# Performance work log

Measured on AMD Instinct MI355X. Metric: run time of the kernel, lower is better.

## Reference

```python
import jax, jax.numpy as jnp
import numpy as np

EMBED_DIM = 1024
NUM_HEADS = 16
HEAD_DIM = EMBED_DIM // NUM_HEADS
B, T = 4, 2048


def setup_inputs() -> dict:
    key = jax.random.key(0)
    ks = jax.random.split(key, 11)
    s = 1.0 / np.sqrt(EMBED_DIM)
    return {
        "query": jax.random.normal(ks[0], (B, T, EMBED_DIM), jnp.float32),
        "key_in": jax.random.normal(ks[1], (B, T, EMBED_DIM), jnp.float32),
        "value": jax.random.normal(ks[2], (B, T, EMBED_DIM), jnp.float32),
        "Wq": jax.random.normal(ks[3], (EMBED_DIM, EMBED_DIM), jnp.float32) * s,
        "bq": jnp.zeros((EMBED_DIM,), jnp.float32),
        "Wk": jax.random.normal(ks[4], (EMBED_DIM, EMBED_DIM), jnp.float32) * s,
        "bk": jnp.zeros((EMBED_DIM,), jnp.float32),
        "Wv": jax.random.normal(ks[5], (EMBED_DIM, EMBED_DIM), jnp.float32) * s,
        "bv": jnp.zeros((EMBED_DIM,), jnp.float32),
        "Wo": jax.random.normal(ks[6], (EMBED_DIM, EMBED_DIM), jnp.float32) * s,
        "bo": jnp.zeros((EMBED_DIM,), jnp.float32),
    }


def reference(query, key_in, value, Wq, bq, Wk, bk, Wv, bv, Wo, bo):
    # nn.Linear: x @ W.T + b
    def split_heads(x):  # [B,T,D] -> [B,H,T,hd]
        return x.reshape(B, T, NUM_HEADS, HEAD_DIM).transpose(0, 2, 1, 3)

    q = split_heads(query @ Wq.T + bq)
    k = split_heads(key_in @ Wk.T + bk)
    v = split_heads(value @ Wv.T + bv)
    scores = jnp.einsum("bhqd,bhkd->bhqk", q, k) / jnp.sqrt(jnp.float32(HEAD_DIM))
    attn = jax.nn.softmax(scores, axis=-1)
    out = jnp.einsum("bhqk,bhkd->bhqd", attn, v)
    out = out.transpose(0, 2, 1, 3).reshape(B, T, EMBED_DIM)
    return out @ Wo.T + bo
```

## Files before the change

kernel.cpp:

```cpp
#include <hip/hip_runtime.h>
#include <hip/hip_bf16.h>
#include <stdint.h>

typedef __bf16 bf16;
typedef __bf16 bf16x8 __attribute__((ext_vector_type(8)));
typedef float f32x4 __attribute__((ext_vector_type(4)));
typedef float f32x16 __attribute__((ext_vector_type(16)));

#define BATCH 4
#define SEQ   2048
#define DIM   1024
#define NH    16
#define HD    64

#define QSCALE 0.18033688011112042f

#define MFMA(a, b, c)   __builtin_amdgcn_mfma_f32_16x16x32_bf16((a), (b), (c), 0, 0, 0)
#define MFMA32(a, b, c) __builtin_amdgcn_mfma_f32_32x32x16_bf16((a), (b), (c), 0, 0, 0)

#define GLOAD16(gsrc, ldst)                                                        \
  __builtin_amdgcn_global_load_lds(                                                \
      (__attribute__((address_space(1))) unsigned int*)(void*)(gsrc),              \
      (__attribute__((address_space(3))) unsigned int*)(ldst), 16, 0, 0)

static __device__ __forceinline__ float fast_exp2(float x) {
#if __has_builtin(__builtin_amdgcn_exp2f)
  return __builtin_amdgcn_exp2f(x);
#else
  return exp2f(x);
#endif
}

__global__ __launch_bounds__(256) void cvt_w_kernel(
    const float* __restrict__ w0, const float* __restrict__ w1,
    const float* __restrict__ w2, const float* __restrict__ w3,
    bf16* __restrict__ o0, bf16* __restrict__ o1,
    bf16* __restrict__ o2, bf16* __restrict__ o3) {
  const float* s;
  bf16* d;
  switch (blockIdx.y) {
    case 0: s = w0; d = o0; break;
    case 1: s = w1; d = o1; break;
    case 2: s = w2; d = o2; break;
    default: s = w3; d = o3; break;
  }
  const int i = (blockIdx.x * 256 + threadIdx.x) * 4;
  const float4 v = *(const float4*)(s + i);
  ushort4 o;
  o.x = __builtin_bit_cast(unsigned short, (bf16)v.x);
  o.y = __builtin_bit_cast(unsigned short, (bf16)v.y);
  o.z = __builtin_bit_cast(unsigned short, (bf16)v.z);
  o.w = __builtin_bit_cast(unsigned short, (bf16)v.w);
  *(ushort4*)((unsigned short*)d + i) = o;
}

__global__ __launch_bounds__(256) void cvt_x_kernel(
    const float* __restrict__ in, bf16* __restrict__ out) {
  const int i = (blockIdx.x * 256 + threadIdx.x) * 8;
  const float4 v0 = *(const float4*)(in + i);
  const float4 v1 = *(const float4*)(in + i + 4);
  bf16x8 p;
  p[0] = (bf16)v0.x; p[1] = (bf16)v0.y; p[2] = (bf16)v0.z; p[3] = (bf16)v0.w;
  p[4] = (bf16)v1.x; p[5] = (bf16)v1.y; p[6] = (bf16)v1.z; p[7] = (bf16)v1.w;
  *(bf16x8*)(out + i) = p;
}

__global__ __launch_bounds__(256, 2) void proj_gemm(
    const bf16* __restrict__ A, const bf16* __restrict__ W,
    const float* __restrict__ bias, bf16* __restrict__ out, int z) {
  __shared__ bf16 Ab[2][128 * 64];
  __shared__ bf16 Bb[2][128 * 64];

  const int tid  = threadIdx.x;
  const int wave = tid >> 6, lane = tid & 63;
  const int r = lane & 15, g = lane >> 4;

  const int wg = blockIdx.x;
  const int sw = ((wg & 7) << 6) | (wg >> 3);
  const int m0 = (sw >> 3) * 128, n0 = (sw & 7) * 128;
  const int wm = (wave >> 1) * 64, wn = (wave & 1) * 64;

  f32x4 acc[4][4] = {};

  const int srr = lane >> 3;
  const int scb = (lane & 7) * 16;
  const int swz = srr << 4;

#define STAGEP(buf, k0)                                                             \
  do {                                                                              \
    _Pragma("unroll") for (int i_ = 0; i_ < 4; ++i_) {                              \
      const int row_ = wave * 32 + i_ * 8 + srr;                                    \
      const char* as_ =                                                             \
          (const char*)(A + (size_t)(m0 + row_) * DIM + (k0)) + (scb ^ swz);        \
      GLOAD16(as_, (char*)&Ab[buf][0] + (wave * 32 + i_ * 8) * 128);                \
      const char* bs_ =                                                             \
          (const char*)(W + (size_t)(n0 + row_) * DIM + (k0)) + (scb ^ swz);        \
      GLOAD16(bs_, (char*)&Bb[buf][0] + (wave * 32 + i_ * 8) * 128);                \
    }                                                                               \
  } while (0)

  STAGEP(0, 0);
  __syncthreads();

  const int NK = DIM / 64;
  for (int it = 0; it < NK; ++it) {
    const int cur = it & 1;
    if (it + 1 < NK) STAGEP(cur ^ 1, (it + 1) * 64);

#pragma unroll
    for (int ks = 0; ks < 2; ++ks) {
      bf16x8 af[4], bfr[4];
#pragma unroll
      for (int mt = 0; mt < 4; ++mt) {
        const int mr = wm + mt * 16 + r;
        af[mt] = *(bf16x8*)((char*)&Ab[cur][0] + mr * 128 +
                            ((ks * 64 + g * 16) ^ ((mr & 7) << 4)));
      }
#pragma unroll
      for (int nt = 0; nt < 4; ++nt) {
        const int nr = wn + nt * 16 + r;
        bfr[nt] = *(bf16x8*)((char*)&Bb[cur][0] + nr * 128 +
                             ((ks * 64 + g * 16) ^ ((nr & 7) << 4)));
      }
#pragma unroll
      for (int mt = 0; mt < 4; ++mt)
#pragma unroll
        for (int nt = 0; nt < 4; ++nt)
          acc[mt][nt] = MFMA(af[mt], bfr[nt], acc[mt][nt]);
    }

    __syncthreads();
  }
#undef STAGEP

  if (z == 2) {
#pragma unroll
    for (int nt = 0; nt < 4; ++nt) {
      const int n = n0 + wn + nt * 16 + r;
      const float bn = bias[n];
#pragma unroll
      for (int mt = 0; mt < 4; ++mt) {
        const int m = m0 + wm + mt * 16 + g * 4;
        const int b = m >> 11, t = m & 2047;
        ushort4 pk;
        pk.x = __builtin_bit_cast(unsigned short, (bf16)(acc[mt][nt][0] + bn));
        pk.y = __builtin_bit_cast(unsigned short, (bf16)(acc[mt][nt][1] + bn));
        pk.z = __builtin_bit_cast(unsigned short, (bf16)(acc[mt][nt][2] + bn));
        pk.w = __builtin_bit_cast(unsigned short, (bf16)(acc[mt][nt][3] + bn));
        *(ushort4*)((unsigned short*)out + (((size_t)(b * DIM + n)) << 11) + t) = pk;
      }
    }
  } else {
    const float scale = (z == 0) ? QSCALE : 1.0f;
#pragma unroll
    for (int mt = 0; mt < 4; ++mt)
#pragma unroll
      for (int nt = 0; nt < 4; ++nt) {
        const int n = n0 + wn + nt * 16 + r;
        const float bn = bias[n];
#pragma unroll
        for (int i = 0; i < 4; ++i) {
          const int m = m0 + wm + mt * 16 + g * 4 + i;
          out[(size_t)m * DIM + n] = (bf16)((acc[mt][nt][i] + bn) * scale);
        }
      }
  }
}

__global__ __launch_bounds__(256, 4) void attn_kernel(
    const bf16* __restrict__ Q, const bf16* __restrict__ K,
    const bf16* __restrict__ Vt, bf16* __restrict__ ctx) {
  __shared__ bf16 Kb[2][64 * 64];
  __shared__ bf16 Vb[2][64 * 64];

  const int tid  = threadIdx.x;
  const int wave = tid >> 6, lane = tid & 63;
  const int l31 = lane & 31, hi = lane >> 5;

  const int wg  = blockIdx.x;
  const int swb = (wg & 7) * 128 + (wg >> 3);
  const int qblk = swb & 15, bh = swb >> 4;
  const int b = bh >> 4, h = bh & 15;
  const int q0 = qblk * 128 + wave * 32;

  bf16x8 qf[4];
  {
    const bf16* qp = Q + ((size_t)(b * SEQ + q0 + l31) * DIM + h * HD);
#pragma unroll
    for (int st = 0; st < 4; ++st)
      qf[st] = *(const bf16x8*)(qp + st * 16 + hi * 8);
  }

  f32x16 accO[2] = {};
  float m_i = -3e38f, l_i = 0.0f;

  const bf16* Kbase = K + (size_t)(b * SEQ) * DIM + h * HD;
  const bf16* Vbase = Vt + (size_t)(b * DIM + h * HD) * SEQ;

  const int srr = lane >> 3;
  const int scb = (lane & 7) * 16;
  const int swz = srr << 4;

  int koff[2], voff[2], kdst[2], vdst[2];
#pragma unroll
  for (int i = 0; i < 2; ++i) {
    const int rl = wave * 16 + i * 8 + srr;
    const int r32 = rl & 31;
    const int t = (r32 >> 2) & 3;
    const int rsrc = (rl & 32) + ((t == 1 || t == 2) ? (r32 ^ 12) : r32);
    koff[i] = rsrc * (DIM * 2) + (scb ^ swz);
    voff[i] = rl * (SEQ * 2) + (scb ^ swz);
    kdst[i] = (wave * 16 + i * 8) * 128;
    vdst[i] = (wave * 16 + i * 8) * 128;
  }

#define STAGE(buf, kv0)                                                             \
  do {                                                                              \
    _Pragma("unroll") for (int i_ = 0; i_ < 2; ++i_) {                              \
      GLOAD16((const char*)Kbase + (size_t)(kv0) * (DIM * 2) + koff[i_],            \
              (char*)&Kb[buf][0] + kdst[i_]);                                       \
      GLOAD16((const char*)Vbase + (size_t)(kv0) * 2 + voff[i_],                    \
              (char*)&Vb[buf][0] + vdst[i_]);                                       \
    }                                                                               \
  } while (0)

  STAGE(0, 0);
  __syncthreads();

  const int NIT = SEQ / 64;
  for (int it = 0; it < NIT; ++it) {
    const int cur = it & 1;
    if (it + 1 < NIT) STAGE(cur ^ 1, (it + 1) * 64);

    f32x16 s[2] = {};
    __builtin_amdgcn_s_setprio(1);
#pragma unroll
    for (int kvt = 0; kvt < 2; ++kvt) {
      const int row = kvt * 32 + l31;
      const char* kb = (const char*)&Kb[cur][0] + row * 128;
      const int rsw = (row & 7) << 4;
#pragma unroll
      for (int st = 0; st < 4; ++st) {
        const bf16x8 kf = *(const bf16x8*)(kb + ((st * 32 + hi * 16) ^ rsw));
        s[kvt] = MFMA32(kf, qf[st], s[kvt]);
      }
    }
    __builtin_amdgcn_s_setprio(0);

    float pm = s[0][0];
#pragma unroll
    for (int kvt = 0; kvt < 2; ++kvt)
#pragma unroll
      for (int e = 0; e < 16; ++e)
        if (kvt || e) pm = fmaxf(pm, s[kvt][e]);
    pm = fmaxf(pm, __shfl_xor(pm, 32));

    if (__any(pm > m_i + 8.0f)) {
      const float mn = fmaxf(m_i, pm);
      const float alpha = fast_exp2(m_i - mn);
      m_i = mn;
      l_i *= alpha;
#pragma unroll
      for (int dt = 0; dt < 2; ++dt)
#pragma unroll
        for (int e = 0; e < 16; ++e) accO[dt][e] *= alpha;
    }

    float rs = 0.0f;
#pragma unroll
    for (int kvt = 0; kvt < 2; ++kvt)
#pragma unroll
      for (int e = 0; e < 16; ++e) {
        s[kvt][e] = fast_exp2(s[kvt][e] - m_i);
        rs += s[kvt][e];
      }
    l_i += rs + __shfl_xor(rs, 32);

    bf16x8 pa[2][2];
#pragma unroll
    for (int kvt = 0; kvt < 2; ++kvt)
#pragma unroll
      for (int kb = 0; kb < 2; ++kb)
#pragma unroll
        for (int j = 0; j < 8; ++j)
          pa[kvt][kb][j] = (bf16)s[kvt][kb * 8 + j];

    __builtin_amdgcn_s_setprio(1);
#pragma unroll
    for (int dt = 0; dt < 2; ++dt) {
      const int row = dt * 32 + l31;
      const char* vb = (const char*)&Vb[cur][0] + row * 128;
      const int rsw = (row & 7) << 4;
#pragma unroll
      for (int kvt = 0; kvt < 2; ++kvt)
#pragma unroll
        for (int kb = 0; kb < 2; ++kb) {
          const bf16x8 vf =
              *(const bf16x8*)(vb + ((kvt * 64 + kb * 32 + hi * 16) ^ rsw));
          accO[dt] = MFMA32(vf, pa[kvt][kb], accO[dt]);
        }
    }
    __builtin_amdgcn_s_setprio(0);

    __syncthreads();
  }
#undef STAGE

  {
    const float inv = 1.0f / l_i;
    bf16* cp = ctx + (size_t)(b * SEQ + q0 + l31) * DIM + h * HD;
#pragma unroll
    for (int dt = 0; dt < 2; ++dt)
#pragma unroll
      for (int rr = 0; rr < 4; ++rr) {
        ushort4 pk;
        pk.x = __builtin_bit_cast(unsigned short, (bf16)(accO[dt][rr * 4 + 0] * inv));
        pk.y = __builtin_bit_cast(unsigned short, (bf16)(accO[dt][rr * 4 + 1] * inv));
        pk.z = __builtin_bit_cast(unsigned short, (bf16)(accO[dt][rr * 4 + 2] * inv));
        pk.w = __builtin_bit_cast(unsigned short, (bf16)(accO[dt][rr * 4 + 3] * inv));
        *(ushort4*)(cp + dt * 32 + rr * 8 + hi * 4) = pk;
      }
  }
}

__global__ __launch_bounds__(256, 2) void out_gemm(
    const bf16* __restrict__ A, const bf16* __restrict__ W,
    const float* __restrict__ bias, float* __restrict__ out) {
  __shared__ bf16 Ab[2][128 * 64];
  __shared__ bf16 Bb[2][128 * 64];

  const int tid  = threadIdx.x;
  const int wave = tid >> 6, lane = tid & 63;
  const int r = lane & 15, g = lane >> 4;

  const int wg = blockIdx.x;
  const int sw = ((wg & 7) << 6) | (wg >> 3);
  const int m0 = (sw >> 3) * 128, n0 = (sw & 7) * 128;
  const int wm = (wave >> 1) * 64, wn = (wave & 1) * 64;

  f32x4 acc[4][4] = {};

  const int srr = lane >> 3;
  const int scb = (lane & 7) * 16;
  const int swz = srr << 4;

#define STAGE2(buf, k0)                                                             \
  do {                                                                              \
    _Pragma("unroll") for (int i_ = 0; i_ < 4; ++i_) {                              \
      const int row_ = wave * 32 + i_ * 8 + srr;                                    \
      const char* as_ =                                                             \
          (const char*)(A + (size_t)(m0 + row_) * DIM + (k0)) + (scb ^ swz);        \
      GLOAD16(as_, (char*)&Ab[buf][0] + (wave * 32 + i_ * 8) * 128);                \
      const char* bs_ =                                                             \
          (const char*)(W + (size_t)(n0 + row_) * DIM + (k0)) + (scb ^ swz);        \
      GLOAD16(bs_, (char*)&Bb[buf][0] + (wave * 32 + i_ * 8) * 128);                \
    }                                                                               \
  } while (0)

  STAGE2(0, 0);
  __syncthreads();

  const int NK = DIM / 64;
  for (int it = 0; it < NK; ++it) {
    const int cur = it & 1;
    if (it + 1 < NK) STAGE2(cur ^ 1, (it + 1) * 64);

#pragma unroll
    for (int ks = 0; ks < 2; ++ks) {
      bf16x8 af[4], bfr[4];
#pragma unroll
      for (int mt = 0; mt < 4; ++mt) {
        const int mr = wm + mt * 16 + r;
        af[mt] = *(bf16x8*)((char*)&Ab[cur][0] + mr * 128 +
                            ((ks * 64 + g * 16) ^ ((mr & 7) << 4)));
      }
#pragma unroll
      for (int nt = 0; nt < 4; ++nt) {
        const int nr = wn + nt * 16 + r;
        bfr[nt] = *(bf16x8*)((char*)&Bb[cur][0] + nr * 128 +
                             ((ks * 64 + g * 16) ^ ((nr & 7) << 4)));
      }
#pragma unroll
      for (int mt = 0; mt < 4; ++mt)
#pragma unroll
        for (int nt = 0; nt < 4; ++nt)
          acc[mt][nt] = MFMA(af[mt], bfr[nt], acc[mt][nt]);
    }

    __syncthreads();
  }
#undef STAGE2

#pragma unroll
  for (int mt = 0; mt < 4; ++mt)
#pragma unroll
    for (int nt = 0; nt < 4; ++nt) {
      const int n = n0 + wn + nt * 16 + r;
      const float bn = bias[n];
#pragma unroll
      for (int i = 0; i < 4; ++i) {
        const int m = m0 + wm + mt * 16 + g * 4 + i;
        out[(size_t)m * DIM + n] = acc[mt][nt][i] + bn;
      }
    }
}

extern "C" void kernel_launch(void* const* d_in, const int* in_sizes, int n_in,
                              void* d_out, int out_size, void* d_ws, size_t ws_size,
                              hipStream_t stream) {
  const float* query  = (const float*)d_in[0];
  const float* key_in = (const float*)d_in[1];
  const float* value  = (const float*)d_in[2];
  const float* Wq = (const float*)d_in[3];
  const float* bq = (const float*)d_in[4];
  const float* Wk = (const float*)d_in[5];
  const float* bk = (const float*)d_in[6];
  const float* Wv = (const float*)d_in[7];
  const float* bv = (const float*)d_in[8];
  const float* Wo = (const float*)d_in[9];
  const float* bo = (const float*)d_in[10];

  char* ws = (char*)d_ws;
  const size_t WSZ = (size_t)DIM * DIM * sizeof(bf16);
  const size_t TSZ = (size_t)BATCH * SEQ * DIM * sizeof(bf16);
  bf16* Wq_b = (bf16*)(ws);
  bf16* Wk_b = (bf16*)(ws + WSZ);
  bf16* Wv_b = (bf16*)(ws + 2 * WSZ);
  bf16* Wo_b = (bf16*)(ws + 3 * WSZ);
  bf16* Q_b  = (bf16*)(ws + 4 * WSZ);
  bf16* K_b  = (bf16*)(ws + 4 * WSZ + TSZ);
  bf16* Vt_b = (bf16*)(ws + 4 * WSZ + 2 * TSZ);
  bf16* C_b  = (bf16*)(ws + 4 * WSZ + 3 * TSZ);
  bf16* X_b  = C_b;

  cvt_w_kernel<<<dim3(DIM * DIM / (256 * 4), 4), 256, 0, stream>>>(
      Wq, Wk, Wv, Wo, Wq_b, Wk_b, Wv_b, Wo_b);

  const int XBLK = BATCH * SEQ * DIM / (256 * 8);

  cvt_x_kernel<<<dim3(XBLK), 256, 0, stream>>>(query, X_b);
  proj_gemm<<<dim3(512), 256, 0, stream>>>(X_b, Wq_b, bq, Q_b, 0);

  cvt_x_kernel<<<dim3(XBLK), 256, 0, stream>>>(key_in, X_b);
  proj_gemm<<<dim3(512), 256, 0, stream>>>(X_b, Wk_b, bk, K_b, 1);

  cvt_x_kernel<<<dim3(XBLK), 256, 0, stream>>>(value, X_b);
  proj_gemm<<<dim3(512), 256, 0, stream>>>(X_b, Wv_b, bv, Vt_b, 2);

  attn_kernel<<<dim3(1024), 256, 0, stream>>>(Q_b, K_b, Vt_b, C_b);

  out_gemm<<<dim3(512), 256, 0, stream>>>(C_b, Wo_b, bo, (float*)d_out);
}
```

Before: 208.1 us.

## Use partial vmcnt waits with raw barriers to overlap next-tile loads

Replaces __syncthreads (which forces a full vmcnt(0) drain) in the QKV projection, attention and output projection loops with explicit s_waitcnt vmcnt(N) plus s_barrier. Each wave waits only for the current buffer's async global-to-LDS loads, so the prefetch of the next tile stays in flight during compute. The softmax row max and row sum are also turned into tree reductions to shorten the dependency chain. This relies on the exact count and ordering of outstanding vector-memory ops, which is fragile if the compiler emits any other loads.

New measurement: 211.3 us. About the same (+1.6%).

```diff
diff --git a/kernel.cpp b/kernel.cpp
--- a/kernel.cpp
+++ b/kernel.cpp
@@ -22,6 +22,13 @@
   __builtin_amdgcn_global_load_lds(                                                \
       (__attribute__((address_space(1))) unsigned int*)(void*)(gsrc),              \
       (__attribute__((address_space(3))) unsigned int*)(ldst), 16, 0, 0)
+
+#define VMCNT0() asm volatile("s_waitcnt vmcnt(0)" ::: "memory")
+#define VMCNT4() asm volatile("s_waitcnt vmcnt(4)" ::: "memory")
+#define VMCNT8() asm volatile("s_waitcnt vmcnt(8)" ::: "memory")
+#define SCHEDBAR() __builtin_amdgcn_sched_barrier(0)
+#define BARRIER()                                                                  \
+  do { SCHEDBAR(); __builtin_amdgcn_s_barrier(); SCHEDBAR(); } while (0)
 
 static __device__ __forceinline__ float fast_exp2(float x) {
 #if __has_builtin(__builtin_amdgcn_exp2f)
@@ -100,12 +107,17 @@
   } while (0)
 
   STAGEP(0, 0);
-  __syncthreads();
 
   const int NK = DIM / 64;
   for (int it = 0; it < NK; ++it) {
     const int cur = it & 1;
-    if (it + 1 < NK) STAGEP(cur ^ 1, (it + 1) * 64);
+    if (it + 1 < NK) {
+      STAGEP(cur ^ 1, (it + 1) * 64);
+      VMCNT8();
+    } else {
+      VMCNT0();
+    }
+    BARRIER();
 
 #pragma unroll
     for (int ks = 0; ks < 2; ++ks) {
@@ -129,7 +141,7 @@
           acc[mt][nt] = MFMA(af[mt], bfr[nt], acc[mt][nt]);
     }
 
-    __syncthreads();
+    if (it + 1 < NK) BARRIER();
   }
 #undef STAGEP
 
@@ -225,12 +237,17 @@
   } while (0)
 
   STAGE(0, 0);
-  __syncthreads();
 
   const int NIT = SEQ / 64;
   for (int it = 0; it < NIT; ++it) {
     const int cur = it & 1;
-    if (it + 1 < NIT) STAGE(cur ^ 1, (it + 1) * 64);
+    if (it + 1 < NIT) {
+      STAGE(cur ^ 1, (it + 1) * 64);
+      VMCNT4();
+    } else {
+      VMCNT0();
+    }
+    BARRIER();
 
     f32x16 s[2] = {};
     __builtin_amdgcn_s_setprio(1);
@@ -247,13 +264,18 @@
     }
     __builtin_amdgcn_s_setprio(0);
 
-    float pm = s[0][0];
-#pragma unroll
-    for (int kvt = 0; kvt < 2; ++kvt)
-#pragma unroll
-      for (int e = 0; e < 16; ++e)
-        if (kvt || e) pm = fmaxf(pm, s[kvt][e]);
-    pm = fmaxf(pm, __shfl_xor(pm, 32));
+    float pm;
+    {
+      f32x16 m16;
+#pragma unroll
+      for (int e = 0; e < 16; ++e) m16[e] = fmaxf(s[0][e], s[1][e]);
+      f32x4 m4;
+#pragma unroll
+      for (int e = 0; e < 4; ++e)
+        m4[e] = fmaxf(fmaxf(m16[e], m16[e + 4]), fmaxf(m16[e + 8], m16[e + 12]));
+      pm = fmaxf(fmaxf(m4[0], m4[1]), fmaxf(m4[2], m4[3]));
+      pm = fmaxf(pm, __shfl_xor(pm, 32));
+    }
 
     if (__any(pm > m_i + 8.0f)) {
       const float mn = fmaxf(m_i, pm);
@@ -266,15 +288,21 @@
         for (int e = 0; e < 16; ++e) accO[dt][e] *= alpha;
     }
 
-    float rs = 0.0f;
 #pragma unroll
     for (int kvt = 0; kvt < 2; ++kvt)
 #pragma unroll
-      for (int e = 0; e < 16; ++e) {
-        s[kvt][e] = fast_exp2(s[kvt][e] - m_i);
-        rs += s[kvt][e];
-      }
-    l_i += rs + __shfl_xor(rs, 32);
+      for (int e = 0; e < 16; ++e) s[kvt][e] = fast_exp2(s[kvt][e] - m_i);
+    {
+      f32x16 t16;
+#pragma unroll
+      for (int e = 0; e < 16; ++e) t16[e] = s[0][e] + s[1][e];
+      f32x4 t4;
+#pragma unroll
+      for (int e = 0; e < 4; ++e)
+        t4[e] = (t16[e] + t16[e + 4]) + (t16[e + 8] + t16[e + 12]);
+      float rs = (t4[0] + t4[1]) + (t4[2] + t4[3]);
+      l_i += rs + __shfl_xor(rs, 32);
+    }
 
     bf16x8 pa[2][2];
 #pragma unroll
@@ -302,7 +330,7 @@
     }
     __builtin_amdgcn_s_setprio(0);
 
-    __syncthreads();
+    if (it + 1 < NIT) BARRIER();
   }
 #undef STAGE
 
@@ -358,12 +386,17 @@
   } while (0)
 
   STAGE2(0, 0);
-  __syncthreads();
 
   const int NK = DIM / 64;
   for (int it = 0; it < NK; ++it) {
     const int cur = it & 1;
-    if (it + 1 < NK) STAGE2(cur ^ 1, (it + 1) * 64);
+    if (it + 1 < NK) {
+      STAGE2(cur ^ 1, (it + 1) * 64);
+      VMCNT8();
+    } else {
+      VMCNT0();
+    }
+    BARRIER();
 
 #pragma unroll
     for (int ks = 0; ks < 2; ++ks) {
@@ -387,7 +420,7 @@
           acc[mt][nt] = MFMA(af[mt], bfr[nt], acc[mt][nt]);
     }
 
-    __syncthreads();
+    if (it + 1 < NK) BARRIER();
   }
 #undef STAGE2
 
```

## Triple-buffer K tiles, store MFMA-fragment LDS layout, and tree-reduce softmax stats

Applied to the files above, without the earlier changes.

The attention kernel now prefetches K two iterations ahead into a 3-slot LDS ring and V one iteration ahead, using explicit vmcnt waits and raw s_barrier in place of a full __syncthreads. LDS tiles are stored pre-arranged in per-lane MFMA fragment order, so each lane reads at lane*16 plus a constant offset with no XOR swizzle arithmetic. The row max and row sum reductions become balanced trees to shorten the dependency chains. LDS use rises from 32 KB to 40 KB per block, which may limit occupancy at 4 blocks per CU, and the hand-written vmcnt counts must match the number of outstanding loads exactly.

New measurement: 218.4 us. 5.0% more time.

```diff
diff --git a/kernel.cpp b/kernel.cpp
--- a/kernel.cpp
+++ b/kernel.cpp
@@ -170,8 +170,8 @@
 __global__ __launch_bounds__(256, 4) void attn_kernel(
     const bf16* __restrict__ Q, const bf16* __restrict__ K,
     const bf16* __restrict__ Vt, bf16* __restrict__ ctx) {
-  __shared__ bf16 Kb[2][64 * 64];
-  __shared__ bf16 Vb[2][64 * 64];
+  __shared__ alignas(16) char Kl[3 * 8192];
+  __shared__ alignas(16) char Vl[2 * 8192];
 
   const int tid  = threadIdx.x;
   const int wave = tid >> 6, lane = tid & 63;
@@ -194,66 +194,84 @@
   f32x16 accO[2] = {};
   float m_i = -3e38f, l_i = 0.0f;
 
-  const bf16* Kbase = K + (size_t)(b * SEQ) * DIM + h * HD;
-  const bf16* Vbase = Vt + (size_t)(b * DIM + h * HD) * SEQ;
-
-  const int srr = lane >> 3;
-  const int scb = (lane & 7) * 16;
-  const int swz = srr << 4;
-
-  int koff[2], voff[2], kdst[2], vdst[2];
+  const char* Kbase = (const char*)(K + (size_t)(b * SEQ) * DIM + h * HD);
+  const char* Vbase = (const char*)(Vt + (size_t)(b * DIM + h * HD) * SEQ);
+
+  const int t_ = (l31 >> 2) & 3;
+  const int pl = (t_ == 1 || t_ == 2) ? (l31 ^ 12) : l31;
+
+  int ksrc[2], kdst[2], vsrc[2], vdst[2];
 #pragma unroll
   for (int i = 0; i < 2; ++i) {
-    const int rl = wave * 16 + i * 8 + srr;
-    const int r32 = rl & 31;
-    const int t = (r32 >> 2) & 3;
-    const int rsrc = (rl & 32) + ((t == 1 || t == 2) ? (r32 ^ 12) : r32);
-    koff[i] = rsrc * (DIM * 2) + (scb ^ swz);
-    voff[i] = rl * (SEQ * 2) + (scb ^ swz);
-    kdst[i] = (wave * 16 + i * 8) * 128;
-    vdst[i] = (wave * 16 + i * 8) * 128;
-  }
-
-#define STAGE(buf, kv0)                                                             \
+    const int ka = wave * 2 + i;
+    const int kvt = ka >> 2, st = ka & 3;
+    ksrc[i] = ((kvt * 32 + pl) * DIM + st * 16 + hi * 8) * 2;
+    kdst[i] = ka * 1024;
+    const int va = wave * 2 + i;
+    const int dt = va >> 2, kvt2 = (va >> 1) & 1, kb = va & 1;
+    vsrc[i] = ((dt * 32 + l31) * SEQ + kvt2 * 32 + kb * 16 + hi * 8) * 2;
+    vdst[i] = va * 1024;
+  }
+
+#define STAGE_K(kbuf, kv0)                                                          \
   do {                                                                              \
-    _Pragma("unroll") for (int i_ = 0; i_ < 2; ++i_) {                              \
-      GLOAD16((const char*)Kbase + (size_t)(kv0) * (DIM * 2) + koff[i_],            \
-              (char*)&Kb[buf][0] + kdst[i_]);                                       \
-      GLOAD16((const char*)Vbase + (size_t)(kv0) * 2 + voff[i_],                    \
-              (char*)&Vb[buf][0] + vdst[i_]);                                       \
-    }                                                                               \
+    _Pragma("unroll") for (int i_ = 0; i_ < 2; ++i_)                                \
+        GLOAD16(Kbase + (size_t)(kv0) * (2 * DIM) + ksrc[i_],                       \
+                Kl + (kbuf) * 8192 + kdst[i_]);                                     \
   } while (0)
-
-  STAGE(0, 0);
-  __syncthreads();
-
+#define STAGE_V(vbuf, kv0)                                                          \
+  do {                                                                              \
+    _Pragma("unroll") for (int i_ = 0; i_ < 2; ++i_)                                \
+        GLOAD16(Vbase + (size_t)(kv0) * 2 + vsrc[i_],                               \
+                Vl + (vbuf) * 8192 + vdst[i_]);                                     \
+  } while (0)
+
+  STAGE_K(0, 0);
+  STAGE_V(0, 0);
+  STAGE_K(1, 64);
+
+  int kc = 0;
+  int kst = 2;
   const int NIT = SEQ / 64;
   for (int it = 0; it < NIT; ++it) {
-    const int cur = it & 1;
-    if (it + 1 < NIT) STAGE(cur ^ 1, (it + 1) * 64);
-
+    const int vcur = it & 1;
+    if (it + 2 < NIT) {
+      STAGE_K(kst, (it + 2) * 64);
+      STAGE_V(vcur ^ 1, (it + 1) * 64);
+      asm volatile("s_waitcnt vmcnt(6)" ::: "memory");
+    } else if (it + 1 < NIT) {
+      STAGE_V(vcur ^ 1, (it + 1) * 64);
+      asm volatile("s_waitcnt vmcnt(4)" ::: "memory");
+    } else {
+      asm volatile("s_waitcnt vmcnt(0)" ::: "memory");
+    }
+    __builtin_amdgcn_s_barrier();
+    asm volatile("" ::: "memory");
+
+    const char* kbp = Kl + kc * 8192 + lane * 16;
     f32x16 s[2] = {};
     __builtin_amdgcn_s_setprio(1);
 #pragma unroll
-    for (int kvt = 0; kvt < 2; ++kvt) {
-      const int row = kvt * 32 + l31;
-      const char* kb = (const char*)&Kb[cur][0] + row * 128;
-      const int rsw = (row & 7) << 4;
+    for (int kvt = 0; kvt < 2; ++kvt)
 #pragma unroll
       for (int st = 0; st < 4; ++st) {
-        const bf16x8 kf = *(const bf16x8*)(kb + ((st * 32 + hi * 16) ^ rsw));
+        const bf16x8 kf = *(const bf16x8*)(kbp + (kvt * 4 + st) * 1024);
         s[kvt] = MFMA32(kf, qf[st], s[kvt]);
       }
-    }
     __builtin_amdgcn_s_setprio(0);
 
-    float pm = s[0][0];
-#pragma unroll
-    for (int kvt = 0; kvt < 2; ++kvt)
-#pragma unroll
-      for (int e = 0; e < 16; ++e)
-        if (kvt || e) pm = fmaxf(pm, s[kvt][e]);
-    pm = fmaxf(pm, __shfl_xor(pm, 32));
+    float pm;
+    {
+      f32x16 m16;
+#pragma unroll
+      for (int e = 0; e < 16; ++e) m16[e] = fmaxf(s[0][e], s[1][e]);
+      f32x4 m4;
+#pragma unroll
+      for (int e = 0; e < 4; ++e)
+        m4[e] = fmaxf(fmaxf(m16[e], m16[e + 4]), fmaxf(m16[e + 8], m16[e + 12]));
+      pm = fmaxf(fmaxf(m4[0], m4[1]), fmaxf(m4[2], m4[3]));
+      pm = fmaxf(pm, __shfl_xor(pm, 32));
+    }
 
     if (__any(pm > m_i + 8.0f)) {
       const float mn = fmaxf(m_i, pm);
@@ -266,15 +284,21 @@
         for (int e = 0; e < 16; ++e) accO[dt][e] *= alpha;
     }
 
-    float rs = 0.0f;
 #pragma unroll
     for (int kvt = 0; kvt < 2; ++kvt)
 #pragma unroll
-      for (int e = 0; e < 16; ++e) {
-        s[kvt][e] = fast_exp2(s[kvt][e] - m_i);
-        rs += s[kvt][e];
-      }
-    l_i += rs + __shfl_xor(rs, 32);
+      for (int e = 0; e < 16; ++e) s[kvt][e] = fast_exp2(s[kvt][e] - m_i);
+    {
+      f32x16 t16;
+#pragma unroll
+      for (int e = 0; e < 16; ++e) t16[e] = s[0][e] + s[1][e];
+      f32x4 t4;
+#pragma unroll
+      for (int e = 0; e < 4; ++e)
+        t4[e] = (t16[e] + t16[e + 4]) + (t16[e + 8] + t16[e + 12]);
+      float rs = (t4[0] + t4[1]) + (t4[2] + t4[3]);
+      l_i += rs + __shfl_xor(rs, 32);
+    }
 
     bf16x8 pa[2][2];
 #pragma unroll
@@ -285,26 +309,30 @@
         for (int j = 0; j < 8; ++j)
           pa[kvt][kb][j] = (bf16)s[kvt][kb * 8 + j];
 
+    const char* vbp = Vl + vcur * 8192 + lane * 16;
     __builtin_amdgcn_s_setprio(1);
 #pragma unroll
-    for (int dt = 0; dt < 2; ++dt) {
-      const int row = dt * 32 + l31;
-      const char* vb = (const char*)&Vb[cur][0] + row * 128;
-      const int rsw = (row & 7) << 4;
+    for (int dt = 0; dt < 2; ++dt)
 #pragma unroll
       for (int kvt = 0; kvt < 2; ++kvt)
 #pragma unroll
         for (int kb = 0; kb < 2; ++kb) {
           const bf16x8 vf =
-              *(const bf16x8*)(vb + ((kvt * 64 + kb * 32 + hi * 16) ^ rsw));
+              *(const bf16x8*)(vbp + (dt * 4 + kvt * 2 + kb) * 1024);
           accO[dt] = MFMA32(vf, pa[kvt][kb], accO[dt]);
         }
-    }
     __builtin_amdgcn_s_setprio(0);
 
-    __syncthreads();
-  }
-#undef STAGE
+    if (it + 1 < NIT) {
+      asm volatile("" ::: "memory");
+      __builtin_amdgcn_s_barrier();
+      asm volatile("" ::: "memory");
+    }
+    kc = (kc == 2) ? 0 : kc + 1;
+    kst = (kst == 2) ? 0 : kst + 1;
+  }
+#undef STAGE_K
+#undef STAGE_V
 
   {
     const float inv = 1.0f / l_i;
```
